# Kernel optimization log

Hardware: AMD Instinct MI355X
Metric: run time of the kernel (lower is better)

Reference implementation:

```python
import jax, jax.numpy as jnp
import numpy as np

B, N, E, H = 16, 577, 1024, 16          # batch, tokens (1 cls + 24x24 patches), embed, heads
HD = E // H
LORA_E, LORA_R = 4, 16                   # LoRA experts, rank
AD_E, AD_D = 4, 64                       # adapter experts, bottleneck
FF = 4 * E


def setup_inputs() -> dict:
    key = jax.random.key(0)
    ks = jax.random.split(key, 12)
    p = lambda i, shape: jax.random.normal(ks[i], shape, dtype=jnp.float32) * 0.02
    return {
        "tokens": jax.random.normal(ks[0], (B, N, E), dtype=jnp.float32),
        "ln1_g": jnp.ones((E,), jnp.float32), "ln1_b": jnp.zeros((E,), jnp.float32),
        "qkv_w": p(1, (3 * E, E)), "qkv_b": jnp.zeros((3 * E,), jnp.float32),
        "proj_w": p(2, (E, E)), "proj_b": jnp.zeros((E,), jnp.float32),
        "lora_gate_w": p(3, (LORA_E, E)),
        "lora_A": p(4, (LORA_E, LORA_R, E)),
        "lora_B": p(5, (LORA_E, 3 * E, LORA_R)),
        "ln2_g": jnp.ones((E,), jnp.float32), "ln2_b": jnp.zeros((E,), jnp.float32),
        "fc1_w": p(6, (FF, E)), "fc1_b": jnp.zeros((FF,), jnp.float32),
        "fc2_w": p(7, (E, FF)), "fc2_b": jnp.zeros((E,), jnp.float32),
        "ad_gate_w": p(8, (AD_E, E)),
        "ad_down_w": p(9, (AD_E, AD_D, E)), "ad_down_b": jnp.zeros((AD_E, AD_D), jnp.float32),
        "ad_up_w": p(10, (AD_E, E, AD_D)), "ad_up_b": jnp.zeros((AD_E, E), jnp.float32),
    }


def _ln(x, g, b):
    m = x.mean(-1, keepdims=True)
    v = ((x - m) ** 2).mean(-1, keepdims=True)
    return (x - m) * jax.lax.rsqrt(v + 1e-6) * g + b


def reference(tokens, ln1_g, ln1_b, qkv_w, qkv_b, proj_w, proj_b,
              lora_gate_w, lora_A, lora_B, ln2_g, ln2_b,
              fc1_w, fc1_b, fc2_w, fc2_b,
              ad_gate_w, ad_down_w, ad_down_b, ad_up_w, ad_up_b):
    # ---- attention with MoE-LoRA delta on fused QKV ----
    normed = _ln(tokens, ln1_g, ln1_b)                      # [B,N,E]
    qkv = normed @ qkv_w.T + qkv_b                          # [B,N,3E]
    gates = jax.nn.softmax(normed @ lora_gate_w.T, axis=-1)  # [B,N,X]
    h = jnp.einsum('bnd,xrd->bnxr', normed, lora_A)         # low-rank down
    delta = jnp.einsum('bnxr,bnx,xor->bno', h, gates, lora_B)  # gate-weighted up
    qkv = (qkv + delta).reshape(B, N, 3, H, HD).transpose(2, 0, 3, 1, 4)
    q, k, v = qkv[0], qkv[1], qkv[2]                        # [B,H,N,hd]
    scores = jnp.einsum('bhqd,bhkd->bhqk', q, k) * (HD ** -0.5)
    probs = jax.nn.softmax(scores, axis=-1)
    ctx = jnp.einsum('bhqk,bhkd->bhqd', probs, v)
    ctx = ctx.transpose(0, 2, 1, 3).reshape(B, N, E)
    tokens = tokens + (ctx @ proj_w.T + proj_b)
    # ---- MLP + MoE adapter branch (shared norm2 input) ----
    mlp_in = _ln(tokens, ln2_g, ln2_b)
    mlp_out = jax.nn.gelu(mlp_in @ fc1_w.T + fc1_b, approximate=False) @ fc2_w.T + fc2_b
    ag = jax.nn.softmax(mlp_in @ ad_gate_w.T, axis=-1)       # [B,N,Xa]
    ah = jax.nn.gelu(jnp.einsum('bnd,xhd->bnxh', mlp_in, ad_down_w) + ad_down_b,
                     approximate=False)
    ad_out = (jnp.einsum('bnxh,bnx,xoh->bno', ah, ag, ad_up_w)
              + jnp.einsum('bnx,xo->bno', ag, ad_up_b))
    return tokens + mlp_out + ad_out
```

## Files before the change

### kernel.cpp

```cpp
#include <hip/hip_runtime.h>
#include <math.h>

#define TOK 9232
#define EMB 1024
#define NQKV 3072
#define FFD 4096
#define NSEQ 577

typedef __bf16 bf16x8 __attribute__((ext_vector_type(8)));
typedef float f32x4 __attribute__((ext_vector_type(4)));
typedef unsigned short ushort8 __attribute__((ext_vector_type(8)));
typedef unsigned short ushort4v __attribute__((ext_vector_type(4)));

typedef __attribute__((address_space(3))) unsigned int lds_u32_t;
typedef const __attribute__((address_space(1))) unsigned int glob_u32_t;

__device__ __forceinline__ void async16(void* lds, const void* g) {
    __builtin_amdgcn_global_load_lds((glob_u32_t*)g, (lds_u32_t*)lds, 16, 0, 0);
}

__device__ __forceinline__ unsigned short f2bf(float f) {
    unsigned int u = __builtin_bit_cast(unsigned int, f);
    u = (u + 0x7fffu + ((u >> 16) & 1u)) >> 16;
    return (unsigned short)u;
}
__device__ __forceinline__ float bf2f(unsigned short s) {
    unsigned int u = ((unsigned int)s) << 16;
    return __builtin_bit_cast(float, u);
}
__device__ __forceinline__ float gelu_exact(float x) {
    return 0.5f * x * (1.0f + erff(x * 0.70710678118654752f));
}

__global__ void k_f32_to_bf16(const float* __restrict__ in, unsigned short* __restrict__ out, int n) {
    int i = blockIdx.x * 256 + threadIdx.x;
    if (i < n) out[i] = f2bf(in[i]);
}
__global__ void k_pack_bcat(const float* __restrict__ Bw, unsigned short* __restrict__ out) {
    int i = blockIdx.x * 256 + threadIdx.x;
    if (i >= 4 * 3072 * 16) return;
    int x = i / (3072 * 16);
    int rem = i - x * (3072 * 16);
    int o = rem >> 4;
    int r = rem & 15;
    out[o * 64 + x * 16 + r] = f2bf(Bw[i]);
}
__global__ void k_pack_u(const float* __restrict__ Uw, unsigned short* __restrict__ out) {
    int i = blockIdx.x * 256 + threadIdx.x;
    if (i >= 4 * 1024 * 64) return;
    int x = i >> 16;
    int o = (i >> 6) & 1023;
    int h = i & 63;
    out[o * 256 + x * 64 + h] = f2bf(Uw[i]);
}

__global__ __launch_bounds__(256) void k_ln_gates(const float* __restrict__ x,
                                                  const float* __restrict__ g,
                                                  const float* __restrict__ b,
                                                  const float* __restrict__ gw,
                                                  unsigned short* __restrict__ out,
                                                  float* __restrict__ gates) {
    int t = blockIdx.x;
    int tid = threadIdx.x;
    const float* xp = x + (size_t)t * EMB;
    float4 v = ((const float4*)xp)[tid];
    float s = v.x + v.y + v.z + v.w;
    float sq = v.x * v.x + v.y * v.y + v.z * v.z + v.w * v.w;
    #pragma unroll
    for (int off = 32; off > 0; off >>= 1) {
        s += __shfl_down(s, off);
        sq += __shfl_down(sq, off);
    }
    __shared__ float red[8];
    if ((tid & 63) == 0) { red[tid >> 6] = s; red[(tid >> 6) + 4] = sq; }
    __syncthreads();
    float S = red[0] + red[1] + red[2] + red[3];
    float SQ = red[4] + red[5] + red[6] + red[7];
    float mean = S * (1.0f / EMB);
    float var = SQ * (1.0f / EMB) - mean * mean;
    float rstd = rsqrtf(var + 1e-6f);
    float4 gv = ((const float4*)g)[tid];
    float4 bv = ((const float4*)b)[tid];
    float n0 = (v.x - mean) * rstd * gv.x + bv.x;
    float n1 = (v.y - mean) * rstd * gv.y + bv.y;
    float n2 = (v.z - mean) * rstd * gv.z + bv.z;
    float n3 = (v.w - mean) * rstd * gv.w + bv.w;
    ushort4v o;
    o[0] = f2bf(n0); o[1] = f2bf(n1); o[2] = f2bf(n2); o[3] = f2bf(n3);
    ((ushort4v*)(out + (size_t)t * EMB))[tid] = o;
    float p[4];
    #pragma unroll
    for (int xx = 0; xx < 4; ++xx) {
        float4 gr = ((const float4*)(gw + xx * EMB))[tid];
        p[xx] = n0 * gr.x + n1 * gr.y + n2 * gr.z + n3 * gr.w;
    }
    #pragma unroll
    for (int off = 32; off > 0; off >>= 1) {
        #pragma unroll
        for (int xx = 0; xx < 4; ++xx) p[xx] += __shfl_down(p[xx], off);
    }
    __shared__ float red2[4][4];
    if ((tid & 63) == 0) {
        #pragma unroll
        for (int xx = 0; xx < 4; ++xx) red2[tid >> 6][xx] = p[xx];
    }
    __syncthreads();
    if (tid == 0) {
        float l[4];
        #pragma unroll
        for (int xx = 0; xx < 4; ++xx) l[xx] = red2[0][xx] + red2[1][xx] + red2[2][xx] + red2[3][xx];
        float m = fmaxf(fmaxf(l[0], l[1]), fmaxf(l[2], l[3]));
        float e[4], ssum = 0.f;
        #pragma unroll
        for (int xx = 0; xx < 4; ++xx) { e[xx] = expf(l[xx] - m); ssum += e[xx]; }
        float inv = 1.0f / ssum;
        #pragma unroll
        for (int xx = 0; xx < 4; ++xx) gates[t * 4 + xx] = e[xx] * inv;
    }
}

__global__ void k_make_hw(const float* __restrict__ gates, const float* __restrict__ lh,
                          unsigned short* __restrict__ hw) {
    int i = blockIdx.x * 256 + threadIdx.x;
    if (i >= TOK * 64) return;
    int t = i >> 6;
    int j = i & 63;
    hw[i] = f2bf(gates[t * 4 + (j >> 4)] * lh[i]);
}

__global__ void k_make_ahw(const float* __restrict__ ag, const float* __restrict__ ahpre,
                           unsigned short* __restrict__ ahw) {
    int i = blockIdx.x * 256 + threadIdx.x;
    if (i >= TOK * 256) return;
    int t = i >> 8;
    int j = i & 255;
    ahw[i] = f2bf(ag[t * 4 + (j >> 6)] * gelu_exact(ahpre[i]));
}

__global__ __launch_bounds__(256) void k_adbias(const float* __restrict__ ag,
                                                const float* __restrict__ upb,
                                                float* __restrict__ tok2) {
    int t = blockIdx.x;
    int tid = threadIdx.x;
    float g0 = ag[t * 4 + 0], g1 = ag[t * 4 + 1], g2 = ag[t * 4 + 2], g3 = ag[t * 4 + 3];
    float4 b0 = ((const float4*)(upb + 0 * EMB))[tid];
    float4 b1 = ((const float4*)(upb + 1 * EMB))[tid];
    float4 b2 = ((const float4*)(upb + 2 * EMB))[tid];
    float4 b3 = ((const float4*)(upb + 3 * EMB))[tid];
    float4 r = ((float4*)(tok2 + (size_t)t * EMB))[tid];
    r.x += g0 * b0.x + g1 * b1.x + g2 * b2.x + g3 * b3.x;
    r.y += g0 * b0.y + g1 * b1.y + g2 * b2.y + g3 * b3.y;
    r.z += g0 * b0.z + g1 * b1.z + g2 * b2.z + g3 * b3.z;
    r.w += g0 * b0.w + g1 * b1.w + g2 * b2.w + g3 * b3.w;
    ((float4*)(tok2 + (size_t)t * EMB))[tid] = r;
}

template<bool GELU, bool BF16OUT>
__global__ __launch_bounds__(256) void k_gemm(
    const unsigned short* __restrict__ A, const unsigned short* __restrict__ W,
    int M, int N, int K,
    const unsigned short* __restrict__ A2, const unsigned short* __restrict__ W2, int K2,
    const float* __restrict__ bias, const float* __restrict__ resid,
    void* __restrict__ Cout, int ldc, int gy)
{
    __shared__ unsigned short As[128][32];
    __shared__ unsigned short Ws[128][32];
    int tid = threadIdx.x;

    int nwg = gridDim.x;
    int orig = blockIdx.x;
    int xcd = orig & 7, lid = orig >> 3;
    int q = nwg >> 3, r = nwg & 7;
    int wg = (xcd < r ? xcd * (q + 1) : r * (q + 1) + (xcd - r) * q) + lid;
    int bm128 = (wg / gy) * 128;
    int bn128 = (wg % gy) * 128;

    int l = tid & 63, w = tid >> 6;
    int wr = w >> 1, wc = w & 1;
    int lr = l & 15, lk = (l >> 4) * 8;
    int srow = l >> 2;
    int sslot = (l & 3) * 8;

    f32x4 acc[4][4];
    #pragma unroll
    for (int m = 0; m < 4; ++m)
        #pragma unroll
        for (int n = 0; n < 4; ++n) acc[m][n] = (f32x4){0.f, 0.f, 0.f, 0.f};

    auto kloop = [&](const unsigned short* __restrict__ Ap,
                     const unsigned short* __restrict__ Wp, int Kc) {
        for (int k0 = 0; k0 < Kc; k0 += 32) {
            #pragma unroll
            for (int i = 0; i < 2; ++i) {
                int row = w * 32 + i * 16 + srow;
                int ra = bm128 + row; if (ra >= M) ra = M - 1;
                async16((char*)&As[0][0] + w * 2048 + i * 1024,
                        Ap + (size_t)ra * Kc + k0 + sslot);
                int rb = bn128 + row; if (rb >= N) rb = N - 1;
                async16((char*)&Ws[0][0] + w * 2048 + i * 1024,
                        Wp + (size_t)rb * Kc + k0 + sslot);
            }
            __syncthreads();
            bf16x8 af[4], bfr[4];
            #pragma unroll
            for (int m = 0; m < 4; ++m) af[m] = *(const bf16x8*)&As[wr * 64 + m * 16 + lr][lk];
            #pragma unroll
            for (int n = 0; n < 4; ++n) bfr[n] = *(const bf16x8*)&Ws[wc * 64 + n * 16 + lr][lk];
            #pragma unroll
            for (int m = 0; m < 4; ++m)
                #pragma unroll
                for (int n = 0; n < 4; ++n)
                    acc[m][n] = __builtin_amdgcn_mfma_f32_16x16x32_bf16(af[m], bfr[n], acc[m][n], 0, 0, 0);
            __syncthreads();
        }
    };
    kloop(A, W, K);
    if (A2) kloop(A2, W2, K2);

    int rb0 = bm128 + wr * 64;
    int cb0 = bn128 + wc * 64;
    #pragma unroll
    for (int n = 0; n < 4; ++n) {
        int col = cb0 + n * 16 + lr;
        if (col >= N) continue;
        float bv = bias ? bias[col] : 0.0f;
        #pragma unroll
        for (int m = 0; m < 4; ++m) {
            #pragma unroll
            for (int rr = 0; rr < 4; ++rr) {
                int row = rb0 + m * 16 + (l >> 4) * 4 + rr;
                if (row >= M) continue;
                float c = acc[m][n][rr] + bv;
                if (GELU) c = gelu_exact(c);
                if (resid) c += resid[(size_t)row * ldc + col];
                if (BF16OUT) ((unsigned short*)Cout)[(size_t)row * ldc + col] = f2bf(c);
                else ((float*)Cout)[(size_t)row * ldc + col] = c;
            }
        }
    }
}

__global__ __launch_bounds__(256) void k_attn(const unsigned short* __restrict__ qkv,
                                              unsigned short* __restrict__ ctx) {
    int bh = blockIdx.x;
    int qt = blockIdx.y;
    int b = bh >> 4, h = bh & 15;
    int tid = threadIdx.x;
    int l = tid & 63;
    int w = tid >> 6;
    int lr = l & 15;
    int lk = (l >> 4) * 8;

    __shared__ unsigned short Qs[64][72];
    __shared__ unsigned short Ks[64][72];
    __shared__ unsigned short Vt[64][72];
    __shared__ unsigned short Ps[64][72];

    const size_t base = (size_t)b * NSEQ * NQKV + (size_t)h * 64;
    int q0 = qt * 64;

    {
        int row = tid >> 2, ds = (tid & 3) * 16;
        int qrow = q0 + row;
        if (qrow < NSEQ) {
            const unsigned short* src = qkv + base + (size_t)qrow * NQKV + ds;
            #pragma unroll
            for (int j = 0; j < 16; ++j) Qs[row][ds + j] = f2bf(bf2f(src[j]) * 0.125f);
        } else {
            #pragma unroll
            for (int j = 0; j < 16; ++j) Qs[row][ds + j] = 0;
        }
    }

    float m_run[4], l_run[4];
    f32x4 o[4];
    #pragma unroll
    for (int r = 0; r < 4; ++r) { m_run[r] = -1e30f; l_run[r] = 0.0f; }
    #pragma unroll
    for (int n = 0; n < 4; ++n) o[n] = (f32x4){0.f, 0.f, 0.f, 0.f};

    for (int kt = 0; kt < 10; ++kt) {
        __syncthreads();
        {
            int row = tid >> 2, ds = (tid & 3) * 16;
            int key = kt * 64 + row;
            if (key < NSEQ) {
                const unsigned short* ksrc = qkv + base + (size_t)key * NQKV + 1024 + ds;
                *(ushort8*)&Ks[row][ds] = *(const ushort8*)ksrc;
                *(ushort8*)&Ks[row][ds + 8] = *(const ushort8*)(ksrc + 8);
                const unsigned short* vsrc = qkv + base + (size_t)key * NQKV + 2048 + ds;
                #pragma unroll
                for (int j = 0; j < 16; ++j) Vt[ds + j][row] = vsrc[j];
            } else {
                ushort8 z = {};
                *(ushort8*)&Ks[row][ds] = z;
                *(ushort8*)&Ks[row][ds + 8] = z;
                #pragma unroll
                for (int j = 0; j < 16; ++j) Vt[ds + j][row] = 0;
            }
        }
        __syncthreads();

        f32x4 s[4];
        #pragma unroll
        for (int n = 0; n < 4; ++n) s[n] = (f32x4){0.f, 0.f, 0.f, 0.f};
        #pragma unroll
        for (int ks = 0; ks < 2; ++ks) {
            bf16x8 qa = *(const bf16x8*)&Qs[w * 16 + lr][ks * 32 + lk];
            #pragma unroll
            for (int n = 0; n < 4; ++n) {
                bf16x8 kb = *(const bf16x8*)&Ks[n * 16 + lr][ks * 32 + lk];
                s[n] = __builtin_amdgcn_mfma_f32_16x16x32_bf16(qa, kb, s[n], 0, 0, 0);
            }
        }
        #pragma unroll
        for (int n = 0; n < 4; ++n) {
            int col = kt * 64 + n * 16 + lr;
            if (col >= NSEQ) {
                #pragma unroll
                for (int r = 0; r < 4; ++r) s[n][r] = -1e30f;
            }
        }
        float tmax[4];
        #pragma unroll
        for (int r = 0; r < 4; ++r)
            tmax[r] = fmaxf(fmaxf(s[0][r], s[1][r]), fmaxf(s[2][r], s[3][r]));
        #pragma unroll
        for (int off = 1; off < 16; off <<= 1) {
            #pragma unroll
            for (int r = 0; r < 4; ++r) tmax[r] = fmaxf(tmax[r], __shfl_xor(tmax[r], off));
        }
        float alpha[4], rs[4];
        #pragma unroll
        for (int r = 0; r < 4; ++r) {
            float mn = fmaxf(m_run[r], tmax[r]);
            alpha[r] = __expf(m_run[r] - mn);
            m_run[r] = mn;
            rs[r] = 0.0f;
        }
        #pragma unroll
        for (int n = 0; n < 4; ++n) {
            #pragma unroll
            for (int r = 0; r < 4; ++r) {
                float p = __expf(s[n][r] - m_run[r]);
                s[n][r] = p;
                rs[r] += p;
            }
        }
        #pragma unroll
        for (int off = 1; off < 16; off <<= 1) {
            #pragma unroll
            for (int r = 0; r < 4; ++r) rs[r] += __shfl_xor(rs[r], off);
        }
        #pragma unroll
        for (int r = 0; r < 4; ++r) l_run[r] = l_run[r] * alpha[r] + rs[r];
        #pragma unroll
        for (int n = 0; n < 4; ++n) {
            #pragma unroll
            for (int r = 0; r < 4; ++r) o[n][r] *= alpha[r];
        }
        #pragma unroll
        for (int n = 0; n < 4; ++n) {
            #pragma unroll
            for (int r = 0; r < 4; ++r)
                Ps[w * 16 + (l >> 4) * 4 + r][n * 16 + lr] = f2bf(s[n][r]);
        }
        __syncthreads();
        #pragma unroll
        for (int ks = 0; ks < 2; ++ks) {
            bf16x8 pa = *(const bf16x8*)&Ps[w * 16 + lr][ks * 32 + lk];
            #pragma unroll
            for (int n = 0; n < 4; ++n) {
                bf16x8 vb = *(const bf16x8*)&Vt[n * 16 + lr][ks * 32 + lk];
                o[n] = __builtin_amdgcn_mfma_f32_16x16x32_bf16(pa, vb, o[n], 0, 0, 0);
            }
        }
    }
    #pragma unroll
    for (int r = 0; r < 4; ++r) {
        int qrow = q0 + w * 16 + (l >> 4) * 4 + r;
        if (qrow < NSEQ) {
            float inv = (l_run[r] > 0.f) ? 1.0f / l_run[r] : 0.0f;
            #pragma unroll
            for (int n = 0; n < 4; ++n)
                ctx[((size_t)b * NSEQ + qrow) * EMB + h * 64 + n * 16 + lr] = f2bf(o[n][r] * inv);
        }
    }
}

extern "C" void kernel_launch(void* const* d_in, const int* in_sizes, int n_in,
                              void* d_out, int out_size, void* d_ws, size_t ws_size,
                              hipStream_t stream) {
    const float* tokens      = (const float*)d_in[0];
    const float* ln1_g       = (const float*)d_in[1];
    const float* ln1_b       = (const float*)d_in[2];
    const float* qkv_w       = (const float*)d_in[3];
    const float* qkv_b       = (const float*)d_in[4];
    const float* proj_w      = (const float*)d_in[5];
    const float* proj_b      = (const float*)d_in[6];
    const float* lora_gate_w = (const float*)d_in[7];
    const float* lora_A      = (const float*)d_in[8];
    const float* lora_B      = (const float*)d_in[9];
    const float* ln2_g       = (const float*)d_in[10];
    const float* ln2_b       = (const float*)d_in[11];
    const float* fc1_w       = (const float*)d_in[12];
    const float* fc1_b       = (const float*)d_in[13];
    const float* fc2_w       = (const float*)d_in[14];
    const float* fc2_b       = (const float*)d_in[15];
    const float* ad_gate_w   = (const float*)d_in[16];
    const float* ad_down_w   = (const float*)d_in[17];
    const float* ad_down_b   = (const float*)d_in[18];
    const float* ad_up_w     = (const float*)d_in[19];
    const float* ad_up_b     = (const float*)d_in[20];

    char* ws = (char*)d_ws;
    size_t off = 0;
    auto alloc = [&](size_t bytes) -> void* {
        void* p = ws + off;
        off += (bytes + 255) & ~(size_t)255;
        return p;
    };

    unsigned short* w_qkv  = (unsigned short*)alloc((size_t)NQKV * EMB * 2);
    unsigned short* w_proj = (unsigned short*)alloc((size_t)EMB * EMB * 2);
    unsigned short* w_fc1  = (unsigned short*)alloc((size_t)FFD * EMB * 2);
    unsigned short* w_fc2  = (unsigned short*)alloc((size_t)EMB * FFD * 2);
    unsigned short* w_acat = (unsigned short*)alloc((size_t)64 * EMB * 2);
    unsigned short* w_bcat = (unsigned short*)alloc((size_t)NQKV * 64 * 2);
    unsigned short* w_dcat = (unsigned short*)alloc((size_t)256 * EMB * 2);
    unsigned short* w_u    = (unsigned short*)alloc((size_t)EMB * 256 * 2);

    unsigned short* u1 = (unsigned short*)alloc((size_t)TOK * EMB * 2);
    char*           u2 = (char*)alloc((size_t)TOK * EMB * 2);
    unsigned short* u3 = (unsigned short*)alloc((size_t)TOK * FFD * 2);
    float* tok2   = (float*)alloc((size_t)TOK * EMB * 4);
    float* lora_h = (float*)alloc((size_t)TOK * 64 * 4);
    unsigned short* hw = (unsigned short*)alloc((size_t)TOK * 64 * 2);
    float* gates = (float*)alloc((size_t)TOK * 4 * 4);
    float* ag    = (float*)alloc((size_t)TOK * 4 * 4);

    unsigned short* normed = u1;
    unsigned short* mlpin  = u1;
    unsigned short* ctx    = (unsigned short*)u2;
    float*          ahpre  = (float*)u2;
    unsigned short* ahw    = (unsigned short*)(u2 + (size_t)TOK * 256 * 4);
    unsigned short* qkv    = u3;
    unsigned short* h1     = u3;

    k_f32_to_bf16<<<(NQKV * EMB + 255) / 256, 256, 0, stream>>>(qkv_w, w_qkv, NQKV * EMB);
    k_f32_to_bf16<<<(EMB * EMB + 255) / 256, 256, 0, stream>>>(proj_w, w_proj, EMB * EMB);
    k_f32_to_bf16<<<(FFD * EMB + 255) / 256, 256, 0, stream>>>(fc1_w, w_fc1, FFD * EMB);
    k_f32_to_bf16<<<(EMB * FFD + 255) / 256, 256, 0, stream>>>(fc2_w, w_fc2, EMB * FFD);
    k_f32_to_bf16<<<(64 * EMB + 255) / 256, 256, 0, stream>>>(lora_A, w_acat, 64 * EMB);
    k_pack_bcat<<<(NQKV * 64 + 255) / 256, 256, 0, stream>>>(lora_B, w_bcat);
    k_f32_to_bf16<<<(256 * EMB + 255) / 256, 256, 0, stream>>>(ad_down_w, w_dcat, 256 * EMB);
    k_pack_u<<<(EMB * 256 + 255) / 256, 256, 0, stream>>>(ad_up_w, w_u);

    k_ln_gates<<<TOK, 256, 0, stream>>>(tokens, ln1_g, ln1_b, lora_gate_w, normed, gates);
    k_gemm<false, false><<<73 * 1, 256, 0, stream>>>(
        normed, w_acat, TOK, 64, EMB, nullptr, nullptr, 0, nullptr, nullptr, lora_h, 64, 1);
    k_make_hw<<<(TOK * 64 + 255) / 256, 256, 0, stream>>>(gates, lora_h, hw);
    k_gemm<false, true><<<73 * 24, 256, 0, stream>>>(
        normed, w_qkv, TOK, NQKV, EMB, hw, w_bcat, 64, qkv_b, nullptr, qkv, NQKV, 24);
    k_attn<<<dim3(256, 10), 256, 0, stream>>>(qkv, ctx);
    k_gemm<false, false><<<73 * 8, 256, 0, stream>>>(
        ctx, w_proj, TOK, EMB, EMB, nullptr, nullptr, 0, proj_b, tokens, tok2, EMB, 8);
    k_ln_gates<<<TOK, 256, 0, stream>>>(tok2, ln2_g, ln2_b, ad_gate_w, mlpin, ag);
    k_gemm<false, false><<<73 * 2, 256, 0, stream>>>(
        mlpin, w_dcat, TOK, 256, EMB, nullptr, nullptr, 0, ad_down_b, nullptr, ahpre, 256, 2);
    k_make_ahw<<<(TOK * 256 + 255) / 256, 256, 0, stream>>>(ag, ahpre, ahw);
    k_adbias<<<TOK, 256, 0, stream>>>(ag, ad_up_b, tok2);
    k_gemm<true, true><<<73 * 32, 256, 0, stream>>>(
        mlpin, w_fc1, TOK, FFD, EMB, nullptr, nullptr, 0, fc1_b, nullptr, h1, FFD, 32);
    k_gemm<false, false><<<73 * 8, 256, 0, stream>>>(
        h1, w_fc2, TOK, EMB, FFD, ahw, w_u, 256, fc2_b, tok2, d_out, EMB, 8);
}
```

Measured before the change: 785.6 us.

## Add 256x256 double-buffered GEMM with swizzled LDS for large projections

Introduces a 512-thread GEMM kernel with 256x256 tiles, K-step 64, double-buffered async global-to-LDS staging, XOR-swizzled LDS layout, and interleaved barriers with MFMA priority hints. It is used for the QKV, proj, fc1 and fc2 GEMMs, including the fused second-K segment. The LoRA up weights and gated activations are zero-padded from 64 to 128 columns so the K2 segment fits the 64-wide K tile. Small GEMMs keep the old 128 kernel. The goal is to raise arithmetic intensity and hide memory latency, at the cost of coarser tiles (37 row tiles, wasted rows) and higher register and LDS pressure.

```diff
diff --git a/kernel.cpp b/kernel.cpp
--- a/kernel.cpp
+++ b/kernel.cpp
@@ -38,12 +38,11 @@
 }
 __global__ void k_pack_bcat(const float* __restrict__ Bw, unsigned short* __restrict__ out) {
     int i = blockIdx.x * 256 + threadIdx.x;
-    if (i >= 4 * 3072 * 16) return;
-    int x = i / (3072 * 16);
-    int rem = i - x * (3072 * 16);
-    int o = rem >> 4;
-    int r = rem & 15;
-    out[o * 64 + x * 16 + r] = f2bf(Bw[i]);
+    if (i >= 3072 * 128) return;
+    int o = i >> 7, j = i & 127;
+    unsigned short v = 0;
+    if (j < 64) { int x = j >> 4, r = j & 15; v = f2bf(Bw[x * 3072 * 16 + o * 16 + r]); }
+    out[i] = v;
 }
 __global__ void k_pack_u(const float* __restrict__ Uw, unsigned short* __restrict__ out) {
     int i = blockIdx.x * 256 + threadIdx.x;
@@ -122,10 +121,10 @@
 __global__ void k_make_hw(const float* __restrict__ gates, const float* __restrict__ lh,
                           unsigned short* __restrict__ hw) {
     int i = blockIdx.x * 256 + threadIdx.x;
-    if (i >= TOK * 64) return;
-    int t = i >> 6;
-    int j = i & 63;
-    hw[i] = f2bf(gates[t * 4 + (j >> 4)] * lh[i]);
+    if (i >= TOK * 128) return;
+    int t = i >> 7;
+    int j = i & 127;
+    hw[i] = (j < 64) ? f2bf(gates[t * 4 + (j >> 4)] * lh[t * 64 + j]) : 0;
 }
 
 __global__ void k_make_ahw(const float* __restrict__ ag, const float* __restrict__ ahpre,
@@ -155,20 +154,188 @@
     ((float4*)(tok2 + (size_t)t * EMB))[tid] = r;
 }
 
+__device__ __forceinline__ void stage_half(
+    const unsigned short* __restrict__ src, int ldk, int kc,
+    int row0, int rmax, unsigned short* lds_half, int w, int l)
+{
+    #pragma unroll
+    for (int j = 0; j < 2; ++j) {
+        int P = j * 8192 + w * 1024 + l * 16;
+        int row = P >> 7;
+        int slot = ((P >> 4) & 7) ^ (row & 7);
+        int r = row0 + row; if (r > rmax) r = rmax;
+        async16((char*)lds_half + j * 8192 + w * 1024,
+                src + (size_t)r * ldk + kc + slot * 8);
+    }
+}
+
+__device__ __forceinline__ bf16x8 lds_frag(const unsigned short* tile, int row, int c0) {
+    int byte = (row << 7) + (c0 << 1);
+    byte ^= (row & 7) << 4;
+    return *(const bf16x8*)((const char*)tile + byte);
+}
+
+#define STAGE_A(s, ht, Pb) do {                                            \
+    int s_ = (s); if (s_ >= KT) s_ = 0;                                    \
+    const unsigned short* sp_; int ldk_, kc_;                              \
+    if (s_ < KT1) { sp_ = A;  ldk_ = K1; kc_ = s_ << 6; }                  \
+    else          { sp_ = A2; ldk_ = K2; kc_ = (s_ - KT1) << 6; }          \
+    stage_half(sp_, ldk_, kc_, bm + (ht) * 128, M - 1,                     \
+               &SA[Pb][(ht) * 128][0], w, l);                              \
+} while (0)
+
+#define STAGE_B(s, ht, Pb) do {                                            \
+    int s_ = (s); if (s_ >= KT) s_ = 0;                                    \
+    const unsigned short* sp_; int ldk_, kc_;                              \
+    if (s_ < KT1) { sp_ = W;  ldk_ = K1; kc_ = s_ << 6; }                  \
+    else          { sp_ = W2; ldk_ = K2; kc_ = (s_ - KT1) << 6; }          \
+    stage_half(sp_, ldk_, kc_, bn + (ht) * 128, N - 1,                     \
+               &SB[Pb][(ht) * 128][0], w, l);                              \
+} while (0)
+
+#define LDA(Pb, MH)                                                        \
+    _Pragma("unroll")                                                      \
+    for (int f_ = 0; f_ < 4; ++f_)                                         \
+        _Pragma("unroll")                                                  \
+        for (int ks_ = 0; ks_ < 2; ++ks_)                                  \
+            a[f_][ks_] = lds_frag(&SA[Pb][0][0],                           \
+                wm * 128 + (MH) * 64 + f_ * 16 + lr, ks_ * 32 + lk8);
+
+#define LDB(Pb, NH, BREG)                                                  \
+    _Pragma("unroll")                                                      \
+    for (int n_ = 0; n_ < 2; ++n_)                                         \
+        _Pragma("unroll")                                                  \
+        for (int ks_ = 0; ks_ < 2; ++ks_)                                  \
+            BREG[n_][ks_] = lds_frag(&SB[Pb][0][0],                        \
+                wn * 64 + (NH) * 32 + n_ * 16 + lr, ks_ * 32 + lk8);
+
+#define MFMA16(MH, NH, BREG)                                               \
+    __builtin_amdgcn_s_setprio(1);                                         \
+    _Pragma("unroll")                                                      \
+    for (int f_ = 0; f_ < 4; ++f_)                                         \
+        _Pragma("unroll")                                                  \
+        for (int n_ = 0; n_ < 2; ++n_)                                     \
+            _Pragma("unroll")                                              \
+            for (int ks_ = 0; ks_ < 2; ++ks_)                              \
+                acc[(MH) * 4 + f_][(NH) * 2 + n_] =                        \
+                    __builtin_amdgcn_mfma_f32_16x16x32_bf16(               \
+                        a[f_][ks_], BREG[n_][ks_],                         \
+                        acc[(MH) * 4 + f_][(NH) * 2 + n_], 0, 0, 0);       \
+    __builtin_amdgcn_s_setprio(0);
+
+#define VMCNT4 asm volatile("s_waitcnt vmcnt(4)" ::: "memory")
+#define BAR __builtin_amdgcn_s_barrier()
+
 template<bool GELU, bool BF16OUT>
-__global__ __launch_bounds__(256) void k_gemm(
+__global__ __launch_bounds__(512, 2) void k_gemm256(
+    const unsigned short* __restrict__ A, const unsigned short* __restrict__ W,
+    int M, int N, int K1,
+    const unsigned short* __restrict__ A2, const unsigned short* __restrict__ W2, int K2,
+    const float* __restrict__ bias, const float* __restrict__ resid,
+    void* __restrict__ Cout, int ldc, int NT)
+{
+    __shared__ unsigned short SA[2][256][64];
+    __shared__ unsigned short SB[2][256][64];
+
+    int tid = threadIdx.x;
+    int l = tid & 63, w = tid >> 6;
+    int wm = w >> 2, wn = w & 3;
+    int lr = l & 15, lk8 = (l >> 4) * 8;
+
+    int nwg = gridDim.x, orig = blockIdx.x;
+    int xcd = orig & 7, lid = orig >> 3;
+    int q = nwg >> 3, r = nwg & 7;
+    int wg = (xcd < r ? xcd * (q + 1) : r * (q + 1) + (xcd - r) * q) + lid;
+    int bm = (wg / NT) * 256;
+    int bn = (wg % NT) * 256;
+
+    int KT1 = K1 >> 6, KT2 = K2 >> 6;
+    int KT = KT1 + KT2;
+
+    f32x4 acc[8][4];
+    #pragma unroll
+    for (int i = 0; i < 8; ++i)
+        #pragma unroll
+        for (int j = 0; j < 4; ++j) acc[i][j] = (f32x4){0.f, 0.f, 0.f, 0.f};
+
+    STAGE_A(0, 0, 0); STAGE_A(0, 1, 0);
+    STAGE_B(0, 0, 0); STAGE_B(0, 1, 0);
+    STAGE_B(1, 0, 1); STAGE_B(1, 1, 1);
+    VMCNT4;
+    BAR;
+
+    bf16x8 a[4][2], b0[2][2], b1[2][2];
+
+    int SI = KT >> 1;
+    #pragma unroll 1
+    for (int i = 0; i < SI; ++i) {
+        int t0 = i * 2;
+        LDA(0, 0); LDB(0, 0, b0);
+        STAGE_A(t0 + 1, 0, 1);
+        BAR; MFMA16(0, 0, b0); BAR;
+
+        LDB(0, 1, b1);
+        STAGE_A(t0 + 1, 1, 1);
+        BAR; MFMA16(0, 1, b1); BAR;
+
+        LDA(0, 1);
+        STAGE_B(t0 + 2, 0, 0);
+        BAR; MFMA16(1, 0, b0); BAR;
+
+        STAGE_B(t0 + 2, 1, 0);
+        VMCNT4;
+        BAR; MFMA16(1, 1, b1); BAR;
+
+        LDA(1, 0); LDB(1, 0, b0);
+        STAGE_A(t0 + 2, 0, 0);
+        BAR; MFMA16(0, 0, b0); BAR;
+
+        LDB(1, 1, b1);
+        STAGE_A(t0 + 2, 1, 0);
+        BAR; MFMA16(0, 1, b1); BAR;
+
+        LDA(1, 1);
+        STAGE_B(t0 + 3, 0, 1);
+        BAR; MFMA16(1, 0, b0); BAR;
+
+        STAGE_B(t0 + 3, 1, 1);
+        VMCNT4;
+        BAR; MFMA16(1, 1, b1); BAR;
+    }
+
+    #pragma unroll
+    for (int G = 0; G < 4; ++G) {
+        int col = bn + wn * 64 + (G >> 1) * 32 + (G & 1) * 16 + lr;
+        float bv = bias ? bias[col] : 0.0f;
+        #pragma unroll
+        for (int F = 0; F < 8; ++F) {
+            int row0 = bm + wm * 128 + (F >> 2) * 64 + (F & 3) * 16 + (l >> 4) * 4;
+            #pragma unroll
+            for (int rr = 0; rr < 4; ++rr) {
+                int row = row0 + rr;
+                if (row < M) {
+                    float c = acc[F][G][rr] + bv;
+                    if (GELU) c = gelu_exact(c);
+                    if (resid) c += resid[(size_t)row * ldc + col];
+                    if (BF16OUT) ((unsigned short*)Cout)[(size_t)row * ldc + col] = f2bf(c);
+                    else ((float*)Cout)[(size_t)row * ldc + col] = c;
+                }
+            }
+        }
+    }
+}
+
+template<bool GELU, bool BF16OUT>
+__global__ __launch_bounds__(256) void k_gemm128(
     const unsigned short* __restrict__ A, const unsigned short* __restrict__ W,
     int M, int N, int K,
-    const unsigned short* __restrict__ A2, const unsigned short* __restrict__ W2, int K2,
     const float* __restrict__ bias, const float* __restrict__ resid,
     void* __restrict__ Cout, int ldc, int gy)
 {
     __shared__ unsigned short As[128][32];
     __shared__ unsigned short Ws[128][32];
     int tid = threadIdx.x;
-
-    int nwg = gridDim.x;
-    int orig = blockIdx.x;
+    int nwg = gridDim.x, orig = blockIdx.x;
     int xcd = orig & 7, lid = orig >> 3;
     int q = nwg >> 3, r = nwg & 7;
     int wg = (xcd < r ? xcd * (q + 1) : r * (q + 1) + (xcd - r) * q) + lid;
@@ -187,35 +354,30 @@
         #pragma unroll
         for (int n = 0; n < 4; ++n) acc[m][n] = (f32x4){0.f, 0.f, 0.f, 0.f};
 
-    auto kloop = [&](const unsigned short* __restrict__ Ap,
-                     const unsigned short* __restrict__ Wp, int Kc) {
-        for (int k0 = 0; k0 < Kc; k0 += 32) {
-            #pragma unroll
-            for (int i = 0; i < 2; ++i) {
-                int row = w * 32 + i * 16 + srow;
-                int ra = bm128 + row; if (ra >= M) ra = M - 1;
-                async16((char*)&As[0][0] + w * 2048 + i * 1024,
-                        Ap + (size_t)ra * Kc + k0 + sslot);
-                int rb = bn128 + row; if (rb >= N) rb = N - 1;
-                async16((char*)&Ws[0][0] + w * 2048 + i * 1024,
-                        Wp + (size_t)rb * Kc + k0 + sslot);
-            }
-            __syncthreads();
-            bf16x8 af[4], bfr[4];
-            #pragma unroll
-            for (int m = 0; m < 4; ++m) af[m] = *(const bf16x8*)&As[wr * 64 + m * 16 + lr][lk];
-            #pragma unroll
-            for (int n = 0; n < 4; ++n) bfr[n] = *(const bf16x8*)&Ws[wc * 64 + n * 16 + lr][lk];
-            #pragma unroll
-            for (int m = 0; m < 4; ++m)
-                #pragma unroll
-                for (int n = 0; n < 4; ++n)
-                    acc[m][n] = __builtin_amdgcn_mfma_f32_16x16x32_bf16(af[m], bfr[n], acc[m][n], 0, 0, 0);
-            __syncthreads();
-        }
-    };
-    kloop(A, W, K);
-    if (A2) kloop(A2, W2, K2);
+    for (int k0 = 0; k0 < K; k0 += 32) {
+        #pragma unroll
+        for (int i = 0; i < 2; ++i) {
+            int row = w * 32 + i * 16 + srow;
+            int ra = bm128 + row; if (ra >= M) ra = M - 1;
+            async16((char*)&As[0][0] + w * 2048 + i * 1024,
+                    A + (size_t)ra * K + k0 + sslot);
+            int rb = bn128 + row; if (rb >= N) rb = N - 1;
+            async16((char*)&Ws[0][0] + w * 2048 + i * 1024,
+                    W + (size_t)rb * K + k0 + sslot);
+        }
+        __syncthreads();
+        bf16x8 af[4], bfr[4];
+        #pragma unroll
+        for (int m = 0; m < 4; ++m) af[m] = *(const bf16x8*)&As[wr * 64 + m * 16 + lr][lk];
+        #pragma unroll
+        for (int n = 0; n < 4; ++n) bfr[n] = *(const bf16x8*)&Ws[wc * 64 + n * 16 + lr][lk];
+        #pragma unroll
+        for (int m = 0; m < 4; ++m)
+            #pragma unroll
+            for (int n = 0; n < 4; ++n)
+                acc[m][n] = __builtin_amdgcn_mfma_f32_16x16x32_bf16(af[m], bfr[n], acc[m][n], 0, 0, 0);
+        __syncthreads();
+    }
 
     int rb0 = bm128 + wr * 64;
     int cb0 = bn128 + wc * 64;
@@ -426,7 +588,7 @@
     unsigned short* w_fc1  = (unsigned short*)alloc((size_t)FFD * EMB * 2);
     unsigned short* w_fc2  = (unsigned short*)alloc((size_t)EMB * FFD * 2);
     unsigned short* w_acat = (unsigned short*)alloc((size_t)64 * EMB * 2);
-    unsigned short* w_bcat = (unsigned short*)alloc((size_t)NQKV * 64 * 2);
+    unsigned short* w_bcat = (unsigned short*)alloc((size_t)NQKV * 128 * 2);
     unsigned short* w_dcat = (unsigned short*)alloc((size_t)256 * EMB * 2);
     unsigned short* w_u    = (unsigned short*)alloc((size_t)EMB * 256 * 2);
 
@@ -435,7 +597,7 @@
     unsigned short* u3 = (unsigned short*)alloc((size_t)TOK * FFD * 2);
     float* tok2   = (float*)alloc((size_t)TOK * EMB * 4);
     float* lora_h = (float*)alloc((size_t)TOK * 64 * 4);
-    unsigned short* hw = (unsigned short*)alloc((size_t)TOK * 64 * 2);
+    unsigned short* hw = (unsigned short*)alloc((size_t)TOK * 128 * 2);
     float* gates = (float*)alloc((size_t)TOK * 4 * 4);
     float* ag    = (float*)alloc((size_t)TOK * 4 * 4);
 
@@ -452,26 +614,26 @@
     k_f32_to_bf16<<<(FFD * EMB + 255) / 256, 256, 0, stream>>>(fc1_w, w_fc1, FFD * EMB);
     k_f32_to_bf16<<<(EMB * FFD + 255) / 256, 256, 0, stream>>>(fc2_w, w_fc2, EMB * FFD);
     k_f32_to_bf16<<<(64 * EMB + 255) / 256, 256, 0, stream>>>(lora_A, w_acat, 64 * EMB);
-    k_pack_bcat<<<(NQKV * 64 + 255) / 256, 256, 0, stream>>>(lora_B, w_bcat);
+    k_pack_bcat<<<(NQKV * 128 + 255) / 256, 256, 0, stream>>>(lora_B, w_bcat);
     k_f32_to_bf16<<<(256 * EMB + 255) / 256, 256, 0, stream>>>(ad_down_w, w_dcat, 256 * EMB);
     k_pack_u<<<(EMB * 256 + 255) / 256, 256, 0, stream>>>(ad_up_w, w_u);
 
     k_ln_gates<<<TOK, 256, 0, stream>>>(tokens, ln1_g, ln1_b, lora_gate_w, normed, gates);
-    k_gemm<false, false><<<73 * 1, 256, 0, stream>>>(
-        normed, w_acat, TOK, 64, EMB, nullptr, nullptr, 0, nullptr, nullptr, lora_h, 64, 1);
-    k_make_hw<<<(TOK * 64 + 255) / 256, 256, 0, stream>>>(gates, lora_h, hw);
-    k_gemm<false, true><<<73 * 24, 256, 0, stream>>>(
-        normed, w_qkv, TOK, NQKV, EMB, hw, w_bcat, 64, qkv_b, nullptr, qkv, NQKV, 24);
+    k_gemm128<false, false><<<73, 256, 0, stream>>>(
+        normed, w_acat, TOK, 64, EMB, nullptr, nullptr, lora_h, 64, 1);
+    k_make_hw<<<(TOK * 128 + 255) / 256, 256, 0, stream>>>(gates, lora_h, hw);
+    k_gemm256<false, true><<<37 * 12, 512, 0, stream>>>(
+        normed, w_qkv, TOK, NQKV, EMB, hw, w_bcat, 128, qkv_b, nullptr, qkv, NQKV, 12);
     k_attn<<<dim3(256, 10), 256, 0, stream>>>(qkv, ctx);
-    k_gemm<false, false><<<73 * 8, 256, 0, stream>>>(
-        ctx, w_proj, TOK, EMB, EMB, nullptr, nullptr, 0, proj_b, tokens, tok2, EMB, 8);
+    k_gemm256<false, false><<<37 * 4, 512, 0, stream>>>(
+        ctx, w_proj, TOK, EMB, EMB, nullptr, nullptr, 0, proj_b, tokens, tok2, EMB, 4);
     k_ln_gates<<<TOK, 256, 0, stream>>>(tok2, ln2_g, ln2_b, ad_gate_w, mlpin, ag);
-    k_gemm<false, false><<<73 * 2, 256, 0, stream>>>(
-        mlpin, w_dcat, TOK, 256, EMB, nullptr, nullptr, 0, ad_down_b, nullptr, ahpre, 256, 2);
+    k_gemm128<false, false><<<73 * 2, 256, 0, stream>>>(
+        mlpin, w_dcat, TOK, 256, EMB, ad_down_b, nullptr, ahpre, 256, 2);
     k_make_ahw<<<(TOK * 256 + 255) / 256, 256, 0, stream>>>(ag, ahpre, ahw);
     k_adbias<<<TOK, 256, 0, stream>>>(ag, ad_up_b, tok2);
-    k_gemm<true, true><<<73 * 32, 256, 0, stream>>>(
-        mlpin, w_fc1, TOK, FFD, EMB, nullptr, nullptr, 0, fc1_b, nullptr, h1, FFD, 32);
-    k_gemm<false, false><<<73 * 8, 256, 0, stream>>>(
-        h1, w_fc2, TOK, EMB, FFD, ahw, w_u, 256, fc2_b, tok2, d_out, EMB, 8);
-}
+    k_gemm256<true, true><<<37 * 16, 512, 0, stream>>>(
+        mlpin, w_fc1, TOK, FFD, EMB, nullptr, nullptr, 0, fc1_b, nullptr, h1, FFD, 16);
+    k_gemm256<false, false><<<37 * 4, 512, 0, stream>>>(
+        h1, w_fc2, TOK, EMB, FFD, ahw, w_u, 256, fc2_b, tok2, d_out, EMB, 4);
+}
```

After: 840.3 us. 1.07x slower.

## Use 256x256 triple-buffered GEMM and concatenate LoRA/adapter operands along K

Applied to the files above, without the earlier changes.

Replaces the 128x128 single-buffered GEMM for the large matmuls with a 512-thread 256x256 tile kernel. The new kernel uses a three-stage async LDS pipeline, an XOR-swizzled LDS layout and raised MFMA priority. The LoRA up-projection and the adapter up-projection are folded into the main QKV and fc2 GEMMs by concatenating activations and weights along K (1088 and 4352), which removes the second k-loop. This targets global-memory reuse and load latency, at the cost of fewer workgroups (tail effects on 37 row tiles) and higher register and LDS pressure.

```diff
diff --git a/kernel.cpp b/kernel.cpp
--- a/kernel.cpp
+++ b/kernel.cpp
@@ -6,6 +6,8 @@
 #define NQKV 3072
 #define FFD 4096
 #define NSEQ 577
+#define KQKV 1088
+#define KFC2 4352
 
 typedef __bf16 bf16x8 __attribute__((ext_vector_type(8)));
 typedef float f32x4 __attribute__((ext_vector_type(4)));
@@ -32,33 +34,31 @@
     return 0.5f * x * (1.0f + erff(x * 0.70710678118654752f));
 }
 
-__global__ void k_f32_to_bf16(const float* __restrict__ in, unsigned short* __restrict__ out, int n) {
+__global__ void k_pack_str(const float* __restrict__ src, unsigned short* __restrict__ dst,
+                           int K, int LD, int tot) {
     int i = blockIdx.x * 256 + threadIdx.x;
-    if (i < n) out[i] = f2bf(in[i]);
+    if (i >= tot) return;
+    int o = i / K, k = i - o * K;
+    dst[(size_t)o * LD + k] = f2bf(src[i]);
 }
 __global__ void k_pack_bcat(const float* __restrict__ Bw, unsigned short* __restrict__ out) {
     int i = blockIdx.x * 256 + threadIdx.x;
-    if (i >= 4 * 3072 * 16) return;
-    int x = i / (3072 * 16);
-    int rem = i - x * (3072 * 16);
-    int o = rem >> 4;
-    int r = rem & 15;
-    out[o * 64 + x * 16 + r] = f2bf(Bw[i]);
+    if (i >= 3072 * 64) return;
+    int o = i >> 6, j = i & 63, x = j >> 4, r = j & 15;
+    out[(size_t)o * KQKV + 1024 + j] = f2bf(Bw[x * 3072 * 16 + o * 16 + r]);
 }
 __global__ void k_pack_u(const float* __restrict__ Uw, unsigned short* __restrict__ out) {
     int i = blockIdx.x * 256 + threadIdx.x;
-    if (i >= 4 * 1024 * 64) return;
-    int x = i >> 16;
-    int o = (i >> 6) & 1023;
-    int h = i & 63;
-    out[o * 256 + x * 64 + h] = f2bf(Uw[i]);
+    if (i >= 1024 * 256) return;
+    int o = i >> 8, j = i & 255, x = j >> 6, h = j & 63;
+    out[(size_t)o * KFC2 + 4096 + j] = f2bf(Uw[x * 65536 + o * 64 + h]);
 }
 
 __global__ __launch_bounds__(256) void k_ln_gates(const float* __restrict__ x,
                                                   const float* __restrict__ g,
                                                   const float* __restrict__ b,
                                                   const float* __restrict__ gw,
-                                                  unsigned short* __restrict__ out,
+                                                  unsigned short* __restrict__ out, int ostride,
                                                   float* __restrict__ gates) {
     int t = blockIdx.x;
     int tid = threadIdx.x;
@@ -87,7 +87,7 @@
     float n3 = (v.w - mean) * rstd * gv.w + bv.w;
     ushort4v o;
     o[0] = f2bf(n0); o[1] = f2bf(n1); o[2] = f2bf(n2); o[3] = f2bf(n3);
-    ((ushort4v*)(out + (size_t)t * EMB))[tid] = o;
+    *(ushort4v*)(out + (size_t)t * ostride + tid * 4) = o;
     float p[4];
     #pragma unroll
     for (int xx = 0; xx < 4; ++xx) {
@@ -120,21 +120,19 @@
 }
 
 __global__ void k_make_hw(const float* __restrict__ gates, const float* __restrict__ lh,
-                          unsigned short* __restrict__ hw) {
+                          unsigned short* __restrict__ ncat) {
     int i = blockIdx.x * 256 + threadIdx.x;
     if (i >= TOK * 64) return;
-    int t = i >> 6;
-    int j = i & 63;
-    hw[i] = f2bf(gates[t * 4 + (j >> 4)] * lh[i]);
+    int t = i >> 6, j = i & 63;
+    ncat[(size_t)t * KQKV + 1024 + j] = f2bf(gates[t * 4 + (j >> 4)] * lh[i]);
 }
 
 __global__ void k_make_ahw(const float* __restrict__ ag, const float* __restrict__ ahpre,
-                           unsigned short* __restrict__ ahw) {
+                           unsigned short* __restrict__ h1cat) {
     int i = blockIdx.x * 256 + threadIdx.x;
     if (i >= TOK * 256) return;
-    int t = i >> 8;
-    int j = i & 255;
-    ahw[i] = f2bf(ag[t * 4 + (j >> 6)] * gelu_exact(ahpre[i]));
+    int t = i >> 8, j = i & 255;
+    h1cat[(size_t)t * KFC2 + 4096 + j] = f2bf(ag[t * 4 + (j >> 6)] * gelu_exact(ahpre[i]));
 }
 
 __global__ __launch_bounds__(256) void k_adbias(const float* __restrict__ ag,
@@ -155,20 +153,136 @@
     ((float4*)(tok2 + (size_t)t * EMB))[tid] = r;
 }
 
+#define VMCNT8 asm volatile("s_waitcnt vmcnt(8)" ::: "memory")
+#define BAR __builtin_amdgcn_s_barrier()
+
 template<bool GELU, bool BF16OUT>
-__global__ __launch_bounds__(256) void k_gemm(
+__global__ __launch_bounds__(512, 2) void k_gemm256(
     const unsigned short* __restrict__ A, const unsigned short* __restrict__ W,
     int M, int N, int K,
-    const unsigned short* __restrict__ A2, const unsigned short* __restrict__ W2, int K2,
     const float* __restrict__ bias, const float* __restrict__ resid,
+    void* __restrict__ Cout, int ldc, int NT)
+{
+    __shared__ unsigned short SA[3][256][32];
+    __shared__ unsigned short SB[3][256][32];
+
+    int tid = threadIdx.x;
+    int l = tid & 63, w = tid >> 6;
+    int wm = w >> 2, wn = w & 3;
+    int lr = l & 15, lk8 = (l >> 4) * 8;
+
+    int nwg = gridDim.x, orig = blockIdx.x;
+    int xcd = orig & 7, lid = orig >> 3;
+    int q = nwg >> 3, r = nwg & 7;
+    int wg = (xcd < r ? xcd * (q + 1) : r * (q + 1) + (xcd - r) * q) + lid;
+    int bm = (wg / NT) * 256;
+    int bn = (wg % NT) * 256;
+
+    int KT = K >> 5;
+
+    const unsigned short *srcA0, *srcA1, *srcB0, *srcB1;
+    {
+        int P0 = w * 1024 + l * 16;
+        int row0 = P0 >> 6, slot0 = ((P0 >> 4) & 3) ^ ((row0 >> 1) & 3);
+        int row1 = row0 + 128, slot1 = ((P0 >> 4) & 3) ^ ((row1 >> 1) & 3);
+        int ra0 = bm + row0; if (ra0 > M - 1) ra0 = M - 1;
+        int ra1 = bm + row1; if (ra1 > M - 1) ra1 = M - 1;
+        int rb0 = bn + row0; if (rb0 > N - 1) rb0 = N - 1;
+        int rb1 = bn + row1; if (rb1 > N - 1) rb1 = N - 1;
+        srcA0 = A + (size_t)ra0 * K + slot0 * 8;
+        srcA1 = A + (size_t)ra1 * K + slot1 * 8;
+        srcB0 = W + (size_t)rb0 * K + slot0 * 8;
+        srcB1 = W + (size_t)rb1 * K + slot1 * 8;
+    }
+
+    f32x4 acc[8][4];
+    #pragma unroll
+    for (int i = 0; i < 8; ++i)
+        #pragma unroll
+        for (int j = 0; j < 4; ++j) acc[i][j] = (f32x4){0.f, 0.f, 0.f, 0.f};
+
+#define STAGE(s_, sb_) do {                                      \
+    unsigned short* da_ = &SA[sb_][0][0] + (w << 9);             \
+    unsigned short* db_ = &SB[sb_][0][0] + (w << 9);             \
+    int ko_ = (s_) << 5;                                         \
+    async16(da_,        srcA0 + ko_);                            \
+    async16(da_ + 4096, srcA1 + ko_);                            \
+    async16(db_,        srcB0 + ko_);                            \
+    async16(db_ + 4096, srcB1 + ko_);                            \
+} while (0)
+
+    STAGE(0, 0);
+    STAGE(1, 1);
+
+    int cb = 0, sb = 2;
+    #pragma unroll 1
+    for (int t = 0; t < KT; ++t) {
+        int s = t + 2; if (s >= KT) s -= KT;
+        STAGE(s, sb);
+        VMCNT8;
+        BAR;
+        bf16x8 a[8], b[4];
+        const char* baseA = (const char*)&SA[cb][0][0];
+        const char* baseB = (const char*)&SB[cb][0][0];
+        #pragma unroll
+        for (int f = 0; f < 8; ++f) {
+            int rw = wm * 128 + f * 16 + lr;
+            int byte = (rw << 6) + ((lk8 << 1) ^ (((rw >> 1) & 3) << 4));
+            a[f] = *(const bf16x8*)(baseA + byte);
+        }
+        #pragma unroll
+        for (int n = 0; n < 4; ++n) {
+            int rw = wn * 64 + n * 16 + lr;
+            int byte = (rw << 6) + ((lk8 << 1) ^ (((rw >> 1) & 3) << 4));
+            b[n] = *(const bf16x8*)(baseB + byte);
+        }
+        __builtin_amdgcn_s_setprio(1);
+        #pragma unroll
+        for (int f = 0; f < 8; ++f)
+            #pragma unroll
+            for (int n = 0; n < 4; ++n)
+                acc[f][n] = __builtin_amdgcn_mfma_f32_16x16x32_bf16(a[f], b[n], acc[f][n], 0, 0, 0);
+        __builtin_amdgcn_s_setprio(0);
+        BAR;
+        cb = (cb == 2) ? 0 : cb + 1;
+        sb = (sb == 2) ? 0 : sb + 1;
+    }
+#undef STAGE
+
+    #pragma unroll
+    for (int n = 0; n < 4; ++n) {
+        int col = bn + wn * 64 + n * 16 + lr;
+        float bv = bias ? bias[col] : 0.0f;
+        #pragma unroll
+        for (int f = 0; f < 8; ++f) {
+            int row0 = bm + wm * 128 + f * 16 + (l >> 4) * 4;
+            #pragma unroll
+            for (int rr = 0; rr < 4; ++rr) {
+                int row = row0 + rr;
+                if (row < M) {
+                    float c = acc[f][n][rr] + bv;
+                    if (GELU) c = gelu_exact(c);
+                    if (resid) c += resid[(size_t)row * ldc + col];
+                    if (BF16OUT) ((unsigned short*)Cout)[(size_t)row * ldc + col] = f2bf(c);
+                    else ((float*)Cout)[(size_t)row * ldc + col] = c;
+                }
+            }
+        }
+    }
+}
+
+template<bool BF16OUT>
+__global__ __launch_bounds__(256) void k_gemm128(
+    const unsigned short* __restrict__ A, int lda,
+    const unsigned short* __restrict__ W,
+    int M, int N, int K,
+    const float* __restrict__ bias,
     void* __restrict__ Cout, int ldc, int gy)
 {
     __shared__ unsigned short As[128][32];
     __shared__ unsigned short Ws[128][32];
     int tid = threadIdx.x;
-
-    int nwg = gridDim.x;
-    int orig = blockIdx.x;
+    int nwg = gridDim.x, orig = blockIdx.x;
     int xcd = orig & 7, lid = orig >> 3;
     int q = nwg >> 3, r = nwg & 7;
     int wg = (xcd < r ? xcd * (q + 1) : r * (q + 1) + (xcd - r) * q) + lid;
@@ -187,35 +301,30 @@
         #pragma unroll
         for (int n = 0; n < 4; ++n) acc[m][n] = (f32x4){0.f, 0.f, 0.f, 0.f};
 
-    auto kloop = [&](const unsigned short* __restrict__ Ap,
-                     const unsigned short* __restrict__ Wp, int Kc) {
-        for (int k0 = 0; k0 < Kc; k0 += 32) {
-            #pragma unroll
-            for (int i = 0; i < 2; ++i) {
-                int row = w * 32 + i * 16 + srow;
-                int ra = bm128 + row; if (ra >= M) ra = M - 1;
-                async16((char*)&As[0][0] + w * 2048 + i * 1024,
-                        Ap + (size_t)ra * Kc + k0 + sslot);
-                int rb = bn128 + row; if (rb >= N) rb = N - 1;
-                async16((char*)&Ws[0][0] + w * 2048 + i * 1024,
-                        Wp + (size_t)rb * Kc + k0 + sslot);
-            }
-            __syncthreads();
-            bf16x8 af[4], bfr[4];
-            #pragma unroll
-            for (int m = 0; m < 4; ++m) af[m] = *(const bf16x8*)&As[wr * 64 + m * 16 + lr][lk];
-            #pragma unroll
-            for (int n = 0; n < 4; ++n) bfr[n] = *(const bf16x8*)&Ws[wc * 64 + n * 16 + lr][lk];
-            #pragma unroll
-            for (int m = 0; m < 4; ++m)
-                #pragma unroll
-                for (int n = 0; n < 4; ++n)
-                    acc[m][n] = __builtin_amdgcn_mfma_f32_16x16x32_bf16(af[m], bfr[n], acc[m][n], 0, 0, 0);
-            __syncthreads();
-        }
-    };
-    kloop(A, W, K);
-    if (A2) kloop(A2, W2, K2);
+    for (int k0 = 0; k0 < K; k0 += 32) {
+        #pragma unroll
+        for (int i = 0; i < 2; ++i) {
+            int row = w * 32 + i * 16 + srow;
+            int ra = bm128 + row; if (ra >= M) ra = M - 1;
+            async16((char*)&As[0][0] + w * 2048 + i * 1024,
+                    A + (size_t)ra * lda + k0 + sslot);
+            int rb = bn128 + row; if (rb >= N) rb = N - 1;
+            async16((char*)&Ws[0][0] + w * 2048 + i * 1024,
+                    W + (size_t)rb * K + k0 + sslot);
+        }
+        __syncthreads();
+        bf16x8 af[4], bfr[4];
+        #pragma unroll
+        for (int m = 0; m < 4; ++m) af[m] = *(const bf16x8*)&As[wr * 64 + m * 16 + lr][lk];
+        #pragma unroll
+        for (int n = 0; n < 4; ++n) bfr[n] = *(const bf16x8*)&Ws[wc * 64 + n * 16 + lr][lk];
+        #pragma unroll
+        for (int m = 0; m < 4; ++m)
+            #pragma unroll
+            for (int n = 0; n < 4; ++n)
+                acc[m][n] = __builtin_amdgcn_mfma_f32_16x16x32_bf16(af[m], bfr[n], acc[m][n], 0, 0, 0);
+        __syncthreads();
+    }
 
     int rb0 = bm128 + wr * 64;
     int cb0 = bn128 + wc * 64;
@@ -231,8 +340,6 @@
                 int row = rb0 + m * 16 + (l >> 4) * 4 + rr;
                 if (row >= M) continue;
                 float c = acc[m][n][rr] + bv;
-                if (GELU) c = gelu_exact(c);
-                if (resid) c += resid[(size_t)row * ldc + col];
                 if (BF16OUT) ((unsigned short*)Cout)[(size_t)row * ldc + col] = f2bf(c);
                 else ((float*)Cout)[(size_t)row * ldc + col] = c;
             }
@@ -421,57 +528,53 @@
         return p;
     };
 
-    unsigned short* w_qkv  = (unsigned short*)alloc((size_t)NQKV * EMB * 2);
-    unsigned short* w_proj = (unsigned short*)alloc((size_t)EMB * EMB * 2);
-    unsigned short* w_fc1  = (unsigned short*)alloc((size_t)FFD * EMB * 2);
-    unsigned short* w_fc2  = (unsigned short*)alloc((size_t)EMB * FFD * 2);
-    unsigned short* w_acat = (unsigned short*)alloc((size_t)64 * EMB * 2);
-    unsigned short* w_bcat = (unsigned short*)alloc((size_t)NQKV * 64 * 2);
-    unsigned short* w_dcat = (unsigned short*)alloc((size_t)256 * EMB * 2);
-    unsigned short* w_u    = (unsigned short*)alloc((size_t)EMB * 256 * 2);
-
-    unsigned short* u1 = (unsigned short*)alloc((size_t)TOK * EMB * 2);
-    char*           u2 = (char*)alloc((size_t)TOK * EMB * 2);
-    unsigned short* u3 = (unsigned short*)alloc((size_t)TOK * FFD * 2);
+    unsigned short* w_qkvcat = (unsigned short*)alloc((size_t)NQKV * KQKV * 2);
+    unsigned short* w_proj   = (unsigned short*)alloc((size_t)EMB * EMB * 2);
+    unsigned short* w_fc1    = (unsigned short*)alloc((size_t)FFD * EMB * 2);
+    unsigned short* w_fc2cat = (unsigned short*)alloc((size_t)EMB * KFC2 * 2);
+    unsigned short* w_acat   = (unsigned short*)alloc((size_t)64 * EMB * 2);
+    unsigned short* w_dcat   = (unsigned short*)alloc((size_t)256 * EMB * 2);
+
+    char* buf1 = (char*)alloc((size_t)TOK * KQKV * 2);
+    char* buf2 = (char*)alloc((size_t)TOK * KFC2 * 2);
+    char* buf3 = (char*)alloc((size_t)TOK * EMB * 2);
     float* tok2   = (float*)alloc((size_t)TOK * EMB * 4);
     float* lora_h = (float*)alloc((size_t)TOK * 64 * 4);
-    unsigned short* hw = (unsigned short*)alloc((size_t)TOK * 64 * 2);
-    float* gates = (float*)alloc((size_t)TOK * 4 * 4);
-    float* ag    = (float*)alloc((size_t)TOK * 4 * 4);
-
-    unsigned short* normed = u1;
-    unsigned short* mlpin  = u1;
-    unsigned short* ctx    = (unsigned short*)u2;
-    float*          ahpre  = (float*)u2;
-    unsigned short* ahw    = (unsigned short*)(u2 + (size_t)TOK * 256 * 4);
-    unsigned short* qkv    = u3;
-    unsigned short* h1     = u3;
-
-    k_f32_to_bf16<<<(NQKV * EMB + 255) / 256, 256, 0, stream>>>(qkv_w, w_qkv, NQKV * EMB);
-    k_f32_to_bf16<<<(EMB * EMB + 255) / 256, 256, 0, stream>>>(proj_w, w_proj, EMB * EMB);
-    k_f32_to_bf16<<<(FFD * EMB + 255) / 256, 256, 0, stream>>>(fc1_w, w_fc1, FFD * EMB);
-    k_f32_to_bf16<<<(EMB * FFD + 255) / 256, 256, 0, stream>>>(fc2_w, w_fc2, EMB * FFD);
-    k_f32_to_bf16<<<(64 * EMB + 255) / 256, 256, 0, stream>>>(lora_A, w_acat, 64 * EMB);
-    k_pack_bcat<<<(NQKV * 64 + 255) / 256, 256, 0, stream>>>(lora_B, w_bcat);
-    k_f32_to_bf16<<<(256 * EMB + 255) / 256, 256, 0, stream>>>(ad_down_w, w_dcat, 256 * EMB);
-    k_pack_u<<<(EMB * 256 + 255) / 256, 256, 0, stream>>>(ad_up_w, w_u);
-
-    k_ln_gates<<<TOK, 256, 0, stream>>>(tokens, ln1_g, ln1_b, lora_gate_w, normed, gates);
-    k_gemm<false, false><<<73 * 1, 256, 0, stream>>>(
-        normed, w_acat, TOK, 64, EMB, nullptr, nullptr, 0, nullptr, nullptr, lora_h, 64, 1);
-    k_make_hw<<<(TOK * 64 + 255) / 256, 256, 0, stream>>>(gates, lora_h, hw);
-    k_gemm<false, true><<<73 * 24, 256, 0, stream>>>(
-        normed, w_qkv, TOK, NQKV, EMB, hw, w_bcat, 64, qkv_b, nullptr, qkv, NQKV, 24);
+    float* gates  = (float*)alloc((size_t)TOK * 4 * 4);
+    float* ag     = (float*)alloc((size_t)TOK * 4 * 4);
+
+    unsigned short* normedcat = (unsigned short*)buf1;
+    unsigned short* mlpin     = (unsigned short*)buf1;
+    unsigned short* qkv       = (unsigned short*)buf2;
+    unsigned short* h1cat     = (unsigned short*)buf2;
+    unsigned short* ctx       = (unsigned short*)buf3;
+    float*          ahpre     = (float*)buf3;
+
+    k_pack_str<<<(NQKV * EMB + 255) / 256, 256, 0, stream>>>(qkv_w, w_qkvcat, EMB, KQKV, NQKV * EMB);
+    k_pack_bcat<<<(NQKV * 64 + 255) / 256, 256, 0, stream>>>(lora_B, w_qkvcat);
+    k_pack_str<<<(EMB * EMB + 255) / 256, 256, 0, stream>>>(proj_w, w_proj, EMB, EMB, EMB * EMB);
+    k_pack_str<<<(FFD * EMB + 255) / 256, 256, 0, stream>>>(fc1_w, w_fc1, EMB, EMB, FFD * EMB);
+    k_pack_str<<<(EMB * FFD + 255) / 256, 256, 0, stream>>>(fc2_w, w_fc2cat, FFD, KFC2, EMB * FFD);
+    k_pack_u<<<(EMB * 256 + 255) / 256, 256, 0, stream>>>(ad_up_w, w_fc2cat);
+    k_pack_str<<<(64 * EMB + 255) / 256, 256, 0, stream>>>(lora_A, w_acat, EMB, EMB, 64 * EMB);
+    k_pack_str<<<(256 * EMB + 255) / 256, 256, 0, stream>>>(ad_down_w, w_dcat, EMB, EMB, 256 * EMB);
+
+    k_ln_gates<<<TOK, 256, 0, stream>>>(tokens, ln1_g, ln1_b, lora_gate_w, normedcat, KQKV, gates);
+    k_gemm128<false><<<73, 256, 0, stream>>>(
+        normedcat, KQKV, w_acat, TOK, 64, EMB, nullptr, lora_h, 64, 1);
+    k_make_hw<<<(TOK * 64 + 255) / 256, 256, 0, stream>>>(gates, lora_h, normedcat);
+    k_gemm256<false, true><<<37 * 12, 512, 0, stream>>>(
+        normedcat, w_qkvcat, TOK, NQKV, KQKV, qkv_b, nullptr, qkv, NQKV, 12);
     k_attn<<<dim3(256, 10), 256, 0, stream>>>(qkv, ctx);
-    k_gemm<false, false><<<73 * 8, 256, 0, stream>>>(
-        ctx, w_proj, TOK, EMB, EMB, nullptr, nullptr, 0, proj_b, tokens, tok2, EMB, 8);
-    k_ln_gates<<<TOK, 256, 0, stream>>>(tok2, ln2_g, ln2_b, ad_gate_w, mlpin, ag);
-    k_gemm<false, false><<<73 * 2, 256, 0, stream>>>(
-        mlpin, w_dcat, TOK, 256, EMB, nullptr, nullptr, 0, ad_down_b, nullptr, ahpre, 256, 2);
-    k_make_ahw<<<(TOK * 256 + 255) / 256, 256, 0, stream>>>(ag, ahpre, ahw);
+    k_gemm256<false, false><<<37 * 4, 512, 0, stream>>>(
+        ctx, w_proj, TOK, EMB, EMB, proj_b, tokens, tok2, EMB, 4);
+    k_ln_gates<<<TOK, 256, 0, stream>>>(tok2, ln2_g, ln2_b, ad_gate_w, mlpin, EMB, ag);
+    k_gemm128<false><<<73 * 2, 256, 0, stream>>>(
+        mlpin, EMB, w_dcat, TOK, 256, EMB, ad_down_b, ahpre, 256, 2);
+    k_make_ahw<<<(TOK * 256 + 255) / 256, 256, 0, stream>>>(ag, ahpre, h1cat);
     k_adbias<<<TOK, 256, 0, stream>>>(ag, ad_up_b, tok2);
-    k_gemm<true, true><<<73 * 32, 256, 0, stream>>>(
-        mlpin, w_fc1, TOK, FFD, EMB, nullptr, nullptr, 0, fc1_b, nullptr, h1, FFD, 32);
-    k_gemm<false, false><<<73 * 8, 256, 0, stream>>>(
-        h1, w_fc2, TOK, EMB, FFD, ahw, w_u, 256, fc2_b, tok2, d_out, EMB, 8);
-}
+    k_gemm256<true, true><<<37 * 16, 512, 0, stream>>>(
+        mlpin, w_fc1, TOK, FFD, EMB, fc1_b, nullptr, h1cat, KFC2, 16);
+    k_gemm256<false, false><<<37 * 4, 512, 0, stream>>>(
+        h1cat, w_fc2cat, TOK, EMB, KFC2, fc2_b, tok2, d_out, EMB, 4);
+}
```

Result: slower. 906.5 us (+15.4%).
